# Kernel tuning notes

Hardware: AMD Instinct MI355X
Metric: run time of the kernel (lower is better)

The kernel has to match this reference:

```python
import jax, jax.numpy as jnp
import numpy as np

N = 50000
E = 800000
IN_CH = 256
HID = 32
HEADS = 4
OUT_CH = 40
NEG_SLOPE = 0.2
BN_EPS = 1e-5


def _gat_conv(x, W, att_src, att_dst, bias, src, dst, num_nodes, concat):
    # x: [N, F_in]; W: [F_in, H*C]; att_src/att_dst: [H, C]
    H, C = att_src.shape
    h = (x @ W).reshape(num_nodes, H, C)            # [N, H, C]
    a_src = (h * att_src[None]).sum(-1)             # [N, H]
    a_dst = (h * att_dst[None]).sum(-1)             # [N, H]
    e = jax.nn.leaky_relu(a_src[src] + a_dst[dst], NEG_SLOPE)  # [Etot, H]
    # segment softmax over incoming edges of each destination node
    m = jax.ops.segment_max(e, dst, num_segments=num_nodes)    # [N, H]
    ex = jnp.exp(e - m[dst])
    s = jax.ops.segment_sum(ex, dst, num_segments=num_nodes)   # [N, H]
    alpha = ex / (s[dst] + 1e-16)                   # [Etot, H]
    out = jax.ops.segment_sum(h[src] * alpha[:, :, None], dst,
                              num_segments=num_nodes)          # [N, H, C]
    out = out.reshape(num_nodes, H * C) if concat else out.mean(axis=1)
    return out + bias


def setup_inputs() -> dict:
    key = jax.random.key(0)
    ks = jax.random.split(key, 12)
    x = jax.random.normal(ks[0], (N, IN_CH), dtype=jnp.float32)
    edge_index = jax.random.randint(ks[1], (2, E), 0, N, dtype=jnp.int64)
    # layer 1: in -> heads*hid, concat
    W1 = jax.random.normal(ks[2], (IN_CH, HEADS * HID), dtype=jnp.float32) * (1.0 / np.sqrt(IN_CH))
    att_src1 = jax.random.normal(ks[3], (HEADS, HID), dtype=jnp.float32) * 0.1
    att_dst1 = jax.random.normal(ks[4], (HEADS, HID), dtype=jnp.float32) * 0.1
    b1 = jnp.zeros((HEADS * HID,), dtype=jnp.float32)
    # batch norm over hidden*heads features
    gamma = jnp.ones((HEADS * HID,), dtype=jnp.float32)
    beta = jnp.zeros((HEADS * HID,), dtype=jnp.float32)
    # layer 2: heads*hid -> out, heads=1, mean (concat=False)
    W2 = jax.random.normal(ks[5], (HEADS * HID, OUT_CH), dtype=jnp.float32) * (1.0 / np.sqrt(HEADS * HID))
    att_src2 = jax.random.normal(ks[6], (1, OUT_CH), dtype=jnp.float32) * 0.1
    att_dst2 = jax.random.normal(ks[7], (1, OUT_CH), dtype=jnp.float32) * 0.1
    b2 = jnp.zeros((OUT_CH,), dtype=jnp.float32)
    return {"x": x, "edge_index": edge_index, "W1": W1, "att_src1": att_src1,
            "att_dst1": att_dst1, "b1": b1, "gamma": gamma, "beta": beta,
            "W2": W2, "att_src2": att_src2, "att_dst2": att_dst2, "b2": b2}


def reference(x, edge_index, W1, att_src1, att_dst1, b1, gamma, beta,
              W2, att_src2, att_dst2, b2):
    num_nodes = x.shape[0]
    loops = jnp.arange(num_nodes, dtype=edge_index.dtype)
    src = jnp.concatenate([edge_index[0], loops])   # add self-loops (PyG default)
    dst = jnp.concatenate([edge_index[1], loops])
    h = _gat_conv(x, W1, att_src1, att_dst1, b1, src, dst, num_nodes, concat=True)
    # BatchNorm over nodes (training-mode batch statistics)
    mu = h.mean(axis=0)
    var = h.var(axis=0)
    h = (h - mu) * jax.lax.rsqrt(var + BN_EPS) * gamma + beta
    h = jax.nn.elu(h)
    out = _gat_conv(h, W2, att_src2, att_dst2, b2, src, dst, num_nodes, concat=False)
    return out
```

## Files before the change

### kernel.cpp

```cpp
#include <hip/hip_runtime.h>

#define NN 50000
#define EE 800000
#define FIN 256
#define F1 128
#define F2 40
#define CAP 48
#define G1B ((NN + 63) / 64)
#define FILLB ((EE + 255) / 256)
#define G1PB 3126
#define G2P0 3125
#define G2P1 ((NN + 63) / 64)
#define LSTR 56

typedef unsigned int u32;
typedef unsigned short u16;
typedef _Float16 h8 __attribute__((ext_vector_type(8)));
typedef float f4 __attribute__((ext_vector_type(4)));

static __device__ __forceinline__ u32 f2bf(float f) {
  u32 u = __float_as_uint(f);
  return (u + 0x7FFFu + ((u >> 16) & 1u)) >> 16;
}
#define BF_LO(u) __uint_as_float((u) << 16)
#define BF_HI(u) __uint_as_float((u) & 0xFFFF0000u)

static __device__ __forceinline__ int sel4i(int a, int b, int c, int d, int k) {
  int lo = (k & 1) ? b : a;
  int hi = (k & 1) ? d : c;
  return (k & 2) ? hi : lo;
}

__global__ __launch_bounds__(256) void g1f_kernel(const float* __restrict__ x,
                                                  const float* __restrict__ W1,
                                                  const float* __restrict__ att_src,
                                                  const float* __restrict__ att_dst,
                                                  u32* __restrict__ h1bf,
                                                  float* __restrict__ a_src,
                                                  float* __restrict__ a_dst,
                                                  const int* __restrict__ ei,
                                                  int* __restrict__ cnt,
                                                  u16* __restrict__ csr) {
  __shared__ __align__(16) _Float16 Alds[64 * LSTR];
  __shared__ __align__(16) _Float16 Blds[128 * LSTR];
  const int t = threadIdx.x;

  if (blockIdx.x >= G1B) {
    int e = (blockIdx.x - G1B) * 256 + t;
    if (e < EE) {
      int src = ei[e];
      int dst = ei[EE + e];
      int p = atomicAdd(cnt + dst, 1);
      if (p < CAP) csr[dst * CAP + p] = (u16)src;
    }
    return;
  }

  const int m0 = blockIdx.x * 64;
  const int l  = t & 63;
  const int w  = t >> 6;
  const int q  = l & 15;
  const int hq = l >> 4;

  const int arow  = t >> 2;
  const int akoff = (t & 3) * 8;
  const int bn    = t & 127;
  const int bkh   = (t >> 7) * 16;

  f4 acc[8] = {};

  float ax[8];
  float bx[16];
  {
    int gr = m0 + arow;
    if (gr < NN) {
      float4 u0 = *(const float4*)(x + (size_t)gr * FIN + akoff);
      float4 u1 = *(const float4*)(x + (size_t)gr * FIN + akoff + 4);
      ax[0] = u0.x; ax[1] = u0.y; ax[2] = u0.z; ax[3] = u0.w;
      ax[4] = u1.x; ax[5] = u1.y; ax[6] = u1.z; ax[7] = u1.w;
    } else {
#pragma unroll
      for (int i = 0; i < 8; ++i) ax[i] = 0.f;
    }
#pragma unroll
    for (int i = 0; i < 16; ++i) bx[i] = W1[(size_t)(bkh + i) * F1 + bn];
  }

  for (int s = 0; s < 8; ++s) {
    __syncthreads();
    {
      h8 av;
#pragma unroll
      for (int i = 0; i < 8; ++i) av[i] = (_Float16)ax[i];
      *(h8*)(Alds + arow * LSTR + akoff) = av;
      h8 bv0, bv1;
#pragma unroll
      for (int i = 0; i < 8; ++i) { bv0[i] = (_Float16)bx[i]; bv1[i] = (_Float16)bx[8 + i]; }
      *(h8*)(Blds + bn * LSTR + bkh) = bv0;
      *(h8*)(Blds + bn * LSTR + bkh + 8) = bv1;
    }
    __syncthreads();
    if (s < 7) {
      int k0 = (s + 1) * 32;
      int gr = m0 + arow;
      if (gr < NN) {
        float4 u0 = *(const float4*)(x + (size_t)gr * FIN + k0 + akoff);
        float4 u1 = *(const float4*)(x + (size_t)gr * FIN + k0 + akoff + 4);
        ax[0] = u0.x; ax[1] = u0.y; ax[2] = u0.z; ax[3] = u0.w;
        ax[4] = u1.x; ax[5] = u1.y; ax[6] = u1.z; ax[7] = u1.w;
      } else {
#pragma unroll
        for (int i = 0; i < 8; ++i) ax[i] = 0.f;
      }
#pragma unroll
      for (int i = 0; i < 16; ++i) bx[i] = W1[(size_t)(k0 + bkh + i) * F1 + bn];
    }
    h8 af = *(const h8*)(Alds + (w * 16 + q) * LSTR + hq * 8);
#pragma unroll
    for (int nf = 0; nf < 8; ++nf) {
      h8 bf = *(const h8*)(Blds + (nf * 16 + q) * LSTR + hq * 8);
      acc[nf] = __builtin_amdgcn_mfma_f32_16x16x32_f16(af, bf, acc[nf], 0, 0, 0);
    }
  }

  u16* h1u = (u16*)h1bf;
#pragma unroll
  for (int nf = 0; nf < 8; ++nf) {
    int ph = nf >> 1;
#pragma unroll
    for (int r = 0; r < 4; ++r) {
      int grow = m0 + w * 16 + hq * 4 + r;
      if (grow < NN)
        h1u[((size_t)ph * NN + grow) * 32 + (nf & 1) * 16 + q] = (u16)f2bf(acc[nf][r]);
    }
  }
  float as8[8], ad8[8];
#pragma unroll
  for (int nf = 0; nf < 8; ++nf) {
    as8[nf] = att_src[nf * 16 + q];
    ad8[nf] = att_dst[nf * 16 + q];
  }
#pragma unroll
  for (int r = 0; r < 4; ++r) {
    float p0 = acc[0][r] * as8[0] + acc[1][r] * as8[1];
    float p1 = acc[2][r] * as8[2] + acc[3][r] * as8[3];
    float p2 = acc[4][r] * as8[4] + acc[5][r] * as8[5];
    float p3 = acc[6][r] * as8[6] + acc[7][r] * as8[7];
    float d0 = acc[0][r] * ad8[0] + acc[1][r] * ad8[1];
    float d1 = acc[2][r] * ad8[2] + acc[3][r] * ad8[3];
    float d2 = acc[4][r] * ad8[4] + acc[5][r] * ad8[5];
    float d3 = acc[6][r] * ad8[6] + acc[7][r] * ad8[7];
#pragma unroll
    for (int off = 1; off < 16; off <<= 1) {
      p0 += __shfl_xor(p0, off); p1 += __shfl_xor(p1, off);
      p2 += __shfl_xor(p2, off); p3 += __shfl_xor(p3, off);
      d0 += __shfl_xor(d0, off); d1 += __shfl_xor(d1, off);
      d2 += __shfl_xor(d2, off); d3 += __shfl_xor(d3, off);
    }
    int grow = m0 + w * 16 + hq * 4 + r;
    if (grow < NN && q < 8) {
      float vs = (q & 2) ? ((q & 1) ? p3 : p2) : ((q & 1) ? p1 : p0);
      float vd = (q & 2) ? ((q & 1) ? d3 : d2) : ((q & 1) ? d1 : d0);
      if (q < 4) a_src[grow * 4 + q] = vs;
      else       a_dst[grow * 4 + (q - 4)] = vd;
    }
  }
}

__global__ __launch_bounds__(256) void gather1_kernel(const int* __restrict__ cnt,
                                                      const u16* __restrict__ csr,
                                                      const float* __restrict__ a_src,
                                                      const float* __restrict__ a_dst,
                                                      const u32* __restrict__ h1bf,
                                                      const float* __restrict__ b1,
                                                      float* __restrict__ h1b,
                                                      float* __restrict__ bnsum,
                                                      float* __restrict__ bnsq) {
  __shared__ float bns[32], bnq[32];
  __shared__ __align__(16) u16 idx[16 * CAP];
  int t = threadIdx.x;
  if (t < 32) { bns[t] = 0.f; bnq[t] = 0.f; }
  int d = blockIdx.x;
  int xcd = d & 7;
  int p = xcd >> 1;
  int nb = ((d >> 3) << 1) + (xcd & 1);
  int base_n = nb * 16;
  bool blk_ok = (nb < 3125);
  if (blk_ok && t < 96)
    ((uint4*)idx)[t] = ((const uint4*)(csr + (size_t)base_n * CAP))[t];
  __syncthreads();
  int n = base_n + (t >> 4);
  int sub = t & 15;
  int g = sub >> 2;
  int l = sub & 3;
  int f0 = p * 32 + l * 8;
  float acc[8] = {0.f, 0.f, 0.f, 0.f, 0.f, 0.f, 0.f, 0.f};
  float ssum = 0.f;
  if (blk_ok) {
    float adst = a_dst[n * 4 + p];
    const u32* hb = h1bf + (size_t)p * NN * 16 + l * 4;
    if (g == 0) {
      float e0 = a_src[n * 4 + p] + adst;
      e0 = e0 > 0.f ? e0 : 0.2f * e0;
      float x0 = __expf(e0);
      uint4 qv = *(const uint4*)(hb + (size_t)n * 16);
      acc[0] = fmaf(x0, BF_LO(qv.x), acc[0]); acc[1] = fmaf(x0, BF_HI(qv.x), acc[1]);
      acc[2] = fmaf(x0, BF_LO(qv.y), acc[2]); acc[3] = fmaf(x0, BF_HI(qv.y), acc[3]);
      acc[4] = fmaf(x0, BF_LO(qv.z), acc[4]); acc[5] = fmaf(x0, BF_HI(qv.z), acc[5]);
      acc[6] = fmaf(x0, BF_LO(qv.w), acc[6]); acc[7] = fmaf(x0, BF_HI(qv.w), acc[7]);
      ssum += x0;
    }
    const u16* lrow = idx + (t >> 4) * CAP;
    int m = cnt[n]; if (m > CAP) m = CAP;
    int sp = (m + 3) >> 2;
    int i = g * sp;
    int end = i + sp; if (end > m) end = m;
    int gb = (t & 63) & ~3;
    for (; i + 3 < end; i += 4) {
      int s0 = lrow[i + 0];
      int s1 = lrow[i + 1];
      int s2 = lrow[i + 2];
      int s3 = lrow[i + 3];
      float av = a_src[sel4i(s0, s1, s2, s3, l) * 4 + p];
      uint4 q0 = *(const uint4*)(hb + (size_t)s0 * 16);
      uint4 q1 = *(const uint4*)(hb + (size_t)s1 * 16);
      uint4 q2 = *(const uint4*)(hb + (size_t)s2 * 16);
      uint4 q3 = *(const uint4*)(hb + (size_t)s3 * 16);
      float e0 = __shfl(av, gb + 0, 64) + adst;
      float e1 = __shfl(av, gb + 1, 64) + adst;
      float e2 = __shfl(av, gb + 2, 64) + adst;
      float e3 = __shfl(av, gb + 3, 64) + adst;
      e0 = e0 > 0.f ? e0 : 0.2f * e0;  float x0 = __expf(e0);
      e1 = e1 > 0.f ? e1 : 0.2f * e1;  float x1 = __expf(e1);
      e2 = e2 > 0.f ? e2 : 0.2f * e2;  float x2 = __expf(e2);
      e3 = e3 > 0.f ? e3 : 0.2f * e3;  float x3 = __expf(e3);
      acc[0] = fmaf(x0, BF_LO(q0.x), acc[0]); acc[1] = fmaf(x0, BF_HI(q0.x), acc[1]);
      acc[2] = fmaf(x0, BF_LO(q0.y), acc[2]); acc[3] = fmaf(x0, BF_HI(q0.y), acc[3]);
      acc[4] = fmaf(x0, BF_LO(q0.z), acc[4]); acc[5] = fmaf(x0, BF_HI(q0.z), acc[5]);
      acc[6] = fmaf(x0, BF_LO(q0.w), acc[6]); acc[7] = fmaf(x0, BF_HI(q0.w), acc[7]);
      acc[0] = fmaf(x1, BF_LO(q1.x), acc[0]); acc[1] = fmaf(x1, BF_HI(q1.x), acc[1]);
      acc[2] = fmaf(x1, BF_LO(q1.y), acc[2]); acc[3] = fmaf(x1, BF_HI(q1.y), acc[3]);
      acc[4] = fmaf(x1, BF_LO(q1.z), acc[4]); acc[5] = fmaf(x1, BF_HI(q1.z), acc[5]);
      acc[6] = fmaf(x1, BF_LO(q1.w), acc[6]); acc[7] = fmaf(x1, BF_HI(q1.w), acc[7]);
      acc[0] = fmaf(x2, BF_LO(q2.x), acc[0]); acc[1] = fmaf(x2, BF_HI(q2.x), acc[1]);
      acc[2] = fmaf(x2, BF_LO(q2.y), acc[2]); acc[3] = fmaf(x2, BF_HI(q2.y), acc[3]);
      acc[4] = fmaf(x2, BF_LO(q2.z), acc[4]); acc[5] = fmaf(x2, BF_HI(q2.z), acc[5]);
      acc[6] = fmaf(x2, BF_LO(q2.w), acc[6]); acc[7] = fmaf(x2, BF_HI(q2.w), acc[7]);
      acc[0] = fmaf(x3, BF_LO(q3.x), acc[0]); acc[1] = fmaf(x3, BF_HI(q3.x), acc[1]);
      acc[2] = fmaf(x3, BF_LO(q3.y), acc[2]); acc[3] = fmaf(x3, BF_HI(q3.y), acc[3]);
      acc[4] = fmaf(x3, BF_LO(q3.z), acc[4]); acc[5] = fmaf(x3, BF_HI(q3.z), acc[5]);
      acc[6] = fmaf(x3, BF_LO(q3.w), acc[6]); acc[7] = fmaf(x3, BF_HI(q3.w), acc[7]);
      ssum += x0 + x1 + x2 + x3;
    }
    for (; i < end; ++i) {
      int s0 = lrow[i];
      float e0 = a_src[s0 * 4 + p] + adst;
      e0 = e0 > 0.f ? e0 : 0.2f * e0;
      float x0 = __expf(e0);
      uint4 qv = *(const uint4*)(hb + (size_t)s0 * 16);
      acc[0] = fmaf(x0, BF_LO(qv.x), acc[0]); acc[1] = fmaf(x0, BF_HI(qv.x), acc[1]);
      acc[2] = fmaf(x0, BF_LO(qv.y), acc[2]); acc[3] = fmaf(x0, BF_HI(qv.y), acc[3]);
      acc[4] = fmaf(x0, BF_LO(qv.z), acc[4]); acc[5] = fmaf(x0, BF_HI(qv.z), acc[5]);
      acc[6] = fmaf(x0, BF_LO(qv.w), acc[6]); acc[7] = fmaf(x0, BF_HI(qv.w), acc[7]);
      ssum += x0;
    }
  }
#pragma unroll
  for (int j = 0; j < 8; ++j) {
    acc[j] += __shfl_xor(acc[j], 4);
    acc[j] += __shfl_xor(acc[j], 8);
  }
  ssum += __shfl_xor(ssum, 4);
  ssum += __shfl_xor(ssum, 8);
  if (blk_ok && g == 0) {
    float inv = 1.f / (ssum + 1e-16f);
    float4 b0 = *(const float4*)(b1 + f0);
    float4 b4 = *(const float4*)(b1 + f0 + 4);
    float o[8];
    o[0] = acc[0] * inv + b0.x; o[1] = acc[1] * inv + b0.y;
    o[2] = acc[2] * inv + b0.z; o[3] = acc[3] * inv + b0.w;
    o[4] = acc[4] * inv + b4.x; o[5] = acc[5] * inv + b4.y;
    o[6] = acc[6] * inv + b4.z; o[7] = acc[7] * inv + b4.w;
    float4 w0 = {o[0], o[1], o[2], o[3]};
    float4 w1 = {o[4], o[5], o[6], o[7]};
    *(float4*)(h1b + (size_t)n * F1 + f0) = w0;
    *(float4*)(h1b + (size_t)n * F1 + f0 + 4) = w1;
    int lb = l * 8;
#pragma unroll
    for (int j = 0; j < 8; ++j) {
      atomicAdd(&bns[lb + j], o[j]);
      atomicAdd(&bnq[lb + j], o[j] * o[j]);
    }
  }
  __syncthreads();
  if (t < 32) {
    atomicAdd(bnsum + p * 32 + t, bns[t]);
    atomicAdd(bnsq + p * 32 + t, bnq[t]);
  }
}

__global__ __launch_bounds__(256) void gemm2_kernel(const float* __restrict__ hpre,
                                                    const float* __restrict__ W2,
                                                    const float* __restrict__ bnsum,
                                                    const float* __restrict__ bnsq,
                                                    const float* __restrict__ gamma,
                                                    const float* __restrict__ beta,
                                                    u16* __restrict__ h2a,
                                                    u16* __restrict__ h2b,
                                                    const float* __restrict__ att_src2,
                                                    const float* __restrict__ att_dst2,
                                                    float* __restrict__ a_src2,
                                                    float* __restrict__ a_dst2) {
  __shared__ float Wlds[128 * 40];
  __shared__ float Alds[16 * 128];
  __shared__ float sc[128], sh[128];
  int t = threadIdx.x;
  for (int i = t; i < 128 * 40; i += 256) Wlds[i] = W2[i];
  if (t < 128) {
    const float invN = 1.f / (float)NN;
    float mu = bnsum[t] * invN;
    float var = bnsq[t] * invN - mu * mu;
    float s = gamma[t] * rsqrtf(var + 1e-5f);
    sc[t] = s;
    sh[t] = beta[t] - mu * s;
  }
  int tr = t >> 3;
  int tc = t & 7;
  float as5[5], ad5[5];
#pragma unroll
  for (int j = 0; j < 5; ++j) { as5[j] = att_src2[tc * 5 + j]; ad5[j] = att_dst2[tc * 5 + j]; }
  int n0 = blockIdx.x * 128;
  int lrow = t >> 1;
  int lkk = (t & 1) * 8;
  float acc[4][5];
#pragma unroll
  for (int i = 0; i < 4; ++i)
#pragma unroll
    for (int j = 0; j < 5; ++j) acc[i][j] = 0.f;

  for (int k0 = 0; k0 < F1; k0 += 16) {
    float av[8];
    int gn = n0 + lrow;
    if (gn < NN) {
      float4 v0 = *(const float4*)(hpre + (size_t)gn * F1 + k0 + lkk);
      float4 v1 = *(const float4*)(hpre + (size_t)gn * F1 + k0 + lkk + 4);
      av[0] = v0.x; av[1] = v0.y; av[2] = v0.z; av[3] = v0.w;
      av[4] = v1.x; av[5] = v1.y; av[6] = v1.z; av[7] = v1.w;
    } else {
#pragma unroll
      for (int j = 0; j < 8; ++j) av[j] = 0.f;
    }
    __syncthreads();
#pragma unroll
    for (int j = 0; j < 8; ++j) {
      int kg = k0 + lkk + j;
      float a = av[j] * sc[kg] + sh[kg];
      a = a > 0.f ? a : (__expf(a) - 1.f);
      Alds[(lkk + j) * 128 + lrow] = a;
    }
    __syncthreads();
#pragma unroll
    for (int k = 0; k < 16; ++k) {
      float4 a4 = *(const float4*)(Alds + k * 128 + tr * 4);
      float aa[4] = {a4.x, a4.y, a4.z, a4.w};
      float w[5];
#pragma unroll
      for (int j = 0; j < 5; ++j) w[j] = Wlds[(k0 + k) * 40 + tc * 5 + j];
#pragma unroll
      for (int i = 0; i < 4; ++i)
#pragma unroll
        for (int j = 0; j < 5; ++j) acc[i][j] = fmaf(aa[i], w[j], acc[i][j]);
    }
  }
#pragma unroll
  for (int i = 0; i < 4; ++i) {
    int gn = n0 + tr * 4 + i;
    if (gn < NN) {
#pragma unroll
      for (int j = 0; j < 5; ++j) {
        int f = tc * 5 + j;
        u16 v = (u16)f2bf(acc[i][j]);
        if (f < 32) h2a[(size_t)gn * 32 + f] = v;
        else        h2b[(size_t)gn * 8 + (f - 32)] = v;
      }
    }
  }
#pragma unroll
  for (int i = 0; i < 4; ++i) {
    float ps = 0.f, pd = 0.f;
#pragma unroll
    for (int j = 0; j < 5; ++j) { ps += acc[i][j] * as5[j]; pd += acc[i][j] * ad5[j]; }
#pragma unroll
    for (int off = 1; off < 8; off <<= 1) {
      ps += __shfl_xor(ps, off);
      pd += __shfl_xor(pd, off);
    }
    if (tc == 0) {
      int gn = n0 + tr * 4 + i;
      if (gn < NN) { a_src2[gn] = ps; a_dst2[gn] = pd; }
    }
  }
}

__global__ __launch_bounds__(256) void gather2_kernel(const int* __restrict__ cnt,
                                                      const u16* __restrict__ csr,
                                                      const float* __restrict__ a_src,
                                                      const float* __restrict__ a_dst,
                                                      const u32* __restrict__ h2a,
                                                      const u32* __restrict__ h2b,
                                                      const float* __restrict__ b2,
                                                      float* __restrict__ out) {
  int t = threadIdx.x;
  int d = blockIdx.x;
  if (d < G2P0) {
    __shared__ __align__(16) u16 idx[16 * CAP];
    int base_n = d * 16;
    if (t < 96)
      ((uint4*)idx)[t] = ((const uint4*)(csr + (size_t)base_n * CAP))[t];
    __syncthreads();
    int n = base_n + (t >> 4);
    int sub = t & 15;
    int g = sub >> 2;
    int l = sub & 3;
    float adst = a_dst[n];
    const u32* hb = h2a + l * 4;
    float acc[8] = {0.f, 0.f, 0.f, 0.f, 0.f, 0.f, 0.f, 0.f};
    float ssum = 0.f;
    if (g == 0) {
      float e0 = a_src[n] + adst;
      e0 = e0 > 0.f ? e0 : 0.2f * e0;
      float x0 = __expf(e0);
      uint4 qv = *(const uint4*)(hb + (size_t)n * 16);
      acc[0] = fmaf(x0, BF_LO(qv.x), acc[0]); acc[1] = fmaf(x0, BF_HI(qv.x), acc[1]);
      acc[2] = fmaf(x0, BF_LO(qv.y), acc[2]); acc[3] = fmaf(x0, BF_HI(qv.y), acc[3]);
      acc[4] = fmaf(x0, BF_LO(qv.z), acc[4]); acc[5] = fmaf(x0, BF_HI(qv.z), acc[5]);
      acc[6] = fmaf(x0, BF_LO(qv.w), acc[6]); acc[7] = fmaf(x0, BF_HI(qv.w), acc[7]);
      ssum += x0;
    }
    const u16* lrow = idx + (t >> 4) * CAP;
    int m = cnt[n]; if (m > CAP) m = CAP;
    int sp = (m + 3) >> 2;
    int i = g * sp;
    int end = i + sp; if (end > m) end = m;
    int gb = (t & 63) & ~3;
    for (; i + 3 < end; i += 4) {
      int s0 = lrow[i + 0];
      int s1 = lrow[i + 1];
      int s2 = lrow[i + 2];
      int s3 = lrow[i + 3];
      float av = a_src[sel4i(s0, s1, s2, s3, l)];
      uint4 q0 = *(const uint4*)(hb + (size_t)s0 * 16);
      uint4 q1 = *(const uint4*)(hb + (size_t)s1 * 16);
      uint4 q2 = *(const uint4*)(hb + (size_t)s2 * 16);
      uint4 q3 = *(const uint4*)(hb + (size_t)s3 * 16);
      float e0 = __shfl(av, gb + 0, 64) + adst;
      float e1 = __shfl(av, gb + 1, 64) + adst;
      float e2 = __shfl(av, gb + 2, 64) + adst;
      float e3 = __shfl(av, gb + 3, 64) + adst;
      e0 = e0 > 0.f ? e0 : 0.2f * e0;  float x0 = __expf(e0);
      e1 = e1 > 0.f ? e1 : 0.2f * e1;  float x1 = __expf(e1);
      e2 = e2 > 0.f ? e2 : 0.2f * e2;  float x2 = __expf(e2);
      e3 = e3 > 0.f ? e3 : 0.2f * e3;  float x3 = __expf(e3);
      acc[0] = fmaf(x0, BF_LO(q0.x), acc[0]); acc[1] = fmaf(x0, BF_HI(q0.x), acc[1]);
      acc[2] = fmaf(x0, BF_LO(q0.y), acc[2]); acc[3] = fmaf(x0, BF_HI(q0.y), acc[3]);
      acc[4] = fmaf(x0, BF_LO(q0.z), acc[4]); acc[5] = fmaf(x0, BF_HI(q0.z), acc[5]);
      acc[6] = fmaf(x0, BF_LO(q0.w), acc[6]); acc[7] = fmaf(x0, BF_HI(q0.w), acc[7]);
      acc[0] = fmaf(x1, BF_LO(q1.x), acc[0]); acc[1] = fmaf(x1, BF_HI(q1.x), acc[1]);
      acc[2] = fmaf(x1, BF_LO(q1.y), acc[2]); acc[3] = fmaf(x1, BF_HI(q1.y), acc[3]);
      acc[4] = fmaf(x1, BF_LO(q1.z), acc[4]); acc[5] = fmaf(x1, BF_HI(q1.z), acc[5]);
      acc[6] = fmaf(x1, BF_LO(q1.w), acc[6]); acc[7] = fmaf(x1, BF_HI(q1.w), acc[7]);
      acc[0] = fmaf(x2, BF_LO(q2.x), acc[0]); acc[1] = fmaf(x2, BF_HI(q2.x), acc[1]);
      acc[2] = fmaf(x2, BF_LO(q2.y), acc[2]); acc[3] = fmaf(x2, BF_HI(q2.y), acc[3]);
      acc[4] = fmaf(x2, BF_LO(q2.z), acc[4]); acc[5] = fmaf(x2, BF_HI(q2.z), acc[5]);
      acc[6] = fmaf(x2, BF_LO(q2.w), acc[6]); acc[7] = fmaf(x2, BF_HI(q2.w), acc[7]);
      acc[0] = fmaf(x3, BF_LO(q3.x), acc[0]); acc[1] = fmaf(x3, BF_HI(q3.x), acc[1]);
      acc[2] = fmaf(x3, BF_LO(q3.y), acc[2]); acc[3] = fmaf(x3, BF_HI(q3.y), acc[3]);
      acc[4] = fmaf(x3, BF_LO(q3.z), acc[4]); acc[5] = fmaf(x3, BF_HI(q3.z), acc[5]);
      acc[6] = fmaf(x3, BF_LO(q3.w), acc[6]); acc[7] = fmaf(x3, BF_HI(q3.w), acc[7]);
      ssum += x0 + x1 + x2 + x3;
    }
    for (; i < end; ++i) {
      int s0 = lrow[i];
      float e0 = a_src[s0] + adst;
      e0 = e0 > 0.f ? e0 : 0.2f * e0;
      float x0 = __expf(e0);
      uint4 qv = *(const uint4*)(hb + (size_t)s0 * 16);
      acc[0] = fmaf(x0, BF_LO(qv.x), acc[0]); acc[1] = fmaf(x0, BF_HI(qv.x), acc[1]);
      acc[2] = fmaf(x0, BF_LO(qv.y), acc[2]); acc[3] = fmaf(x0, BF_HI(qv.y), acc[3]);
      acc[4] = fmaf(x0, BF_LO(qv.z), acc[4]); acc[5] = fmaf(x0, BF_HI(qv.z), acc[5]);
      acc[6] = fmaf(x0, BF_LO(qv.w), acc[6]); acc[7] = fmaf(x0, BF_HI(qv.w), acc[7]);
      ssum += x0;
    }
#pragma unroll
    for (int j = 0; j < 8; ++j) {
      acc[j] += __shfl_xor(acc[j], 4);
      acc[j] += __shfl_xor(acc[j], 8);
    }
    ssum += __shfl_xor(ssum, 4);
    ssum += __shfl_xor(ssum, 8);
    if (g == 0) {
      float inv = 1.f / (ssum + 1e-16f);
      int f0 = l * 8;
      float4 b0 = *(const float4*)(b2 + f0);
      float4 b4 = *(const float4*)(b2 + f0 + 4);
      float4 w0 = {acc[0] * inv + b0.x, acc[1] * inv + b0.y,
                   acc[2] * inv + b0.z, acc[3] * inv + b0.w};
      float4 w1 = {acc[4] * inv + b4.x, acc[5] * inv + b4.y,
                   acc[6] * inv + b4.z, acc[7] * inv + b4.w};
      *(float4*)(out + (size_t)n * F2 + f0) = w0;
      *(float4*)(out + (size_t)n * F2 + f0 + 4) = w1;
    }
  } else {
    int n = (d - G2P0) * 64 + (t >> 2);
    int g = t & 3;
    float acc[8] = {0.f, 0.f, 0.f, 0.f, 0.f, 0.f, 0.f, 0.f};
    float ssum = 0.f;
    if (n < NN) {
      float adst = a_dst[n];
      if (g == 0) {
        float e0 = a_src[n] + adst;
        e0 = e0 > 0.f ? e0 : 0.2f * e0;
        float x0 = __expf(e0);
        uint4 qv = *(const uint4*)(h2b + (size_t)n * 4);
        acc[0] = fmaf(x0, BF_LO(qv.x), acc[0]); acc[1] = fmaf(x0, BF_HI(qv.x), acc[1]);
        acc[2] = fmaf(x0, BF_LO(qv.y), acc[2]); acc[3] = fmaf(x0, BF_HI(qv.y), acc[3]);
        acc[4] = fmaf(x0, BF_LO(qv.z), acc[4]); acc[5] = fmaf(x0, BF_HI(qv.z), acc[5]);
        acc[6] = fmaf(x0, BF_LO(qv.w), acc[6]); acc[7] = fmaf(x0, BF_HI(qv.w), acc[7]);
        ssum += x0;
      }
      const u16* row = csr + (size_t)n * CAP;
      int m = cnt[n]; if (m > CAP) m = CAP;
      int i = g;
      for (; i + 4 < m; i += 8) {
        int s0 = row[i];
        int s1 = row[i + 4];
        float e0 = a_src[s0];
        float e1 = a_src[s1];
        uint4 q0 = *(const uint4*)(h2b + (size_t)s0 * 4);
        uint4 q1 = *(const uint4*)(h2b + (size_t)s1 * 4);
        e0 += adst; e0 = e0 > 0.f ? e0 : 0.2f * e0;  float x0 = __expf(e0);
        e1 += adst; e1 = e1 > 0.f ? e1 : 0.2f * e1;  float x1 = __expf(e1);
        acc[0] = fmaf(x0, BF_LO(q0.x), acc[0]); acc[1] = fmaf(x0, BF_HI(q0.x), acc[1]);
        acc[2] = fmaf(x0, BF_LO(q0.y), acc[2]); acc[3] = fmaf(x0, BF_HI(q0.y), acc[3]);
        acc[4] = fmaf(x0, BF_LO(q0.z), acc[4]); acc[5] = fmaf(x0, BF_HI(q0.z), acc[5]);
        acc[6] = fmaf(x0, BF_LO(q0.w), acc[6]); acc[7] = fmaf(x0, BF_HI(q0.w), acc[7]);
        acc[0] = fmaf(x1, BF_LO(q1.x), acc[0]); acc[1] = fmaf(x1, BF_HI(q1.x), acc[1]);
        acc[2] = fmaf(x1, BF_LO(q1.y), acc[2]); acc[3] = fmaf(x1, BF_HI(q1.y), acc[3]);
        acc[4] = fmaf(x1, BF_LO(q1.z), acc[4]); acc[5] = fmaf(x1, BF_HI(q1.z), acc[5]);
        acc[6] = fmaf(x1, BF_LO(q1.w), acc[6]); acc[7] = fmaf(x1, BF_HI(q1.w), acc[7]);
        ssum += x0 + x1;
      }
      for (; i < m; i += 4) {
        int s0 = row[i];
        float e0 = a_src[s0] + adst;
        e0 = e0 > 0.f ? e0 : 0.2f * e0;
        float x0 = __expf(e0);
        uint4 qv = *(const uint4*)(h2b + (size_t)s0 * 4);
        acc[0] = fmaf(x0, BF_LO(qv.x), acc[0]); acc[1] = fmaf(x0, BF_HI(qv.x), acc[1]);
        acc[2] = fmaf(x0, BF_LO(qv.y), acc[2]); acc[3] = fmaf(x0, BF_HI(qv.y), acc[3]);
        acc[4] = fmaf(x0, BF_LO(qv.z), acc[4]); acc[5] = fmaf(x0, BF_HI(qv.z), acc[5]);
        acc[6] = fmaf(x0, BF_LO(qv.w), acc[6]); acc[7] = fmaf(x0, BF_HI(qv.w), acc[7]);
        ssum += x0;
      }
    }
#pragma unroll
    for (int j = 0; j < 8; ++j) {
      acc[j] += __shfl_xor(acc[j], 1);
      acc[j] += __shfl_xor(acc[j], 2);
    }
    ssum += __shfl_xor(ssum, 1);
    ssum += __shfl_xor(ssum, 2);
    if (n < NN && g == 0) {
      float inv = 1.f / (ssum + 1e-16f);
      float4 b0 = *(const float4*)(b2 + 32);
      float4 b4 = *(const float4*)(b2 + 36);
      float4 w0 = {acc[0] * inv + b0.x, acc[1] * inv + b0.y,
                   acc[2] * inv + b0.z, acc[3] * inv + b0.w};
      float4 w1 = {acc[4] * inv + b4.x, acc[5] * inv + b4.y,
                   acc[6] * inv + b4.z, acc[7] * inv + b4.w};
      *(float4*)(out + (size_t)n * F2 + 32) = w0;
      *(float4*)(out + (size_t)n * F2 + 36) = w1;
    }
  }
}

extern "C" void kernel_launch(void* const* d_in, const int* in_sizes, int n_in,
                              void* d_out, int out_size, void* d_ws, size_t ws_size,
                              hipStream_t stream) {
  const float* x        = (const float*)d_in[0];
  const int*   ei       = (const int*)d_in[1];
  const float* W1       = (const float*)d_in[2];
  const float* att_src1 = (const float*)d_in[3];
  const float* att_dst1 = (const float*)d_in[4];
  const float* b1       = (const float*)d_in[5];
  const float* gamma    = (const float*)d_in[6];
  const float* beta     = (const float*)d_in[7];
  const float* W2       = (const float*)d_in[8];
  const float* att_src2 = (const float*)d_in[9];
  const float* att_dst2 = (const float*)d_in[10];
  const float* b2       = (const float*)d_in[11];
  float* out = (float*)d_out;

  int* cnt      = (int*)d_ws;
  float* bnsum  = (float*)(cnt + 50048);
  float* bnsq   = bnsum + 128;
  u16* csr      = (u16*)(bnsq + 128);
  u32* h1bf     = (u32*)(csr + (size_t)NN * CAP);
  float* h1b    = (float*)(h1bf + 3200000);
  u32* h2a      = (u32*)(h1b + 6400000);
  u32* h2b      = h2a + 800000;
  float* a_src1 = (float*)(h2b + 200000);
  float* a_dst1 = a_src1 + 200000;
  float* a_src2 = a_dst1 + 200000;
  float* a_dst2 = a_src2 + 50000;

  hipMemsetAsync(cnt, 0, (50048 + 256) * sizeof(int), stream);

  g1f_kernel<<<G1B + FILLB, 256, 0, stream>>>(x, W1, att_src1, att_dst1,
                                              h1bf, a_src1, a_dst1,
                                              ei, cnt, csr);
  gather1_kernel<<<(G1PB / 2) * 8, 256, 0, stream>>>(cnt, csr, a_src1, a_dst1,
                                                     h1bf, b1, h1b, bnsum, bnsq);
  gemm2_kernel<<<(NN + 127) / 128, 256, 0, stream>>>(h1b, W2, bnsum, bnsq,
                                                     gamma, beta,
                                                     (u16*)h2a, (u16*)h2b,
                                                     att_src2, att_dst2,
                                                     a_src2, a_dst2);
  gather2_kernel<<<G2P0 + G2P1, 256, 0, stream>>>(cnt, csr, a_src2, a_dst2,
                                                  h2a, h2b, b2, out);
}
```

Before: 287.8 us.

## Merge second-layer gather paths and pack tail features with source attention score

The second-layer gather previously ran two separate block populations: one covering the first 32 output features and one covering the last 8, each walking the CSR rows and recomputing attention weights. It now uses a single pass in which each lane also loads a 32-byte record holding the 8 tail features plus the a_src score, and accumulates those tail features alongside the main ones. This removes the duplicate edge traversal, exp computation and extra blocks, and replaces a separate a_src gather with a load that also brings in the tail features. In exchange, per-thread register use and memory traffic grow slightly, and a layout is added that stores the score inside the bf16 row padding.

```diff
diff --git a/kernel.cpp b/kernel.cpp
--- a/kernel.cpp
+++ b/kernel.cpp
@@ -9,8 +9,7 @@
 #define G1B ((NN + 63) / 64)
 #define FILLB ((EE + 255) / 256)
 #define G1PB 3126
-#define G2P0 3125
-#define G2P1 ((NN + 63) / 64)
+#define G2B 3125
 #define LSTR 56
 
 typedef unsigned int u32;
@@ -28,6 +27,11 @@
 static __device__ __forceinline__ int sel4i(int a, int b, int c, int d, int k) {
   int lo = (k & 1) ? b : a;
   int hi = (k & 1) ? d : c;
+  return (k & 2) ? hi : lo;
+}
+static __device__ __forceinline__ float sel4f(float a, float b, float c, float d, int k) {
+  float lo = (k & 1) ? b : a;
+  float hi = (k & 1) ? d : c;
   return (k & 2) ? hi : lo;
 }
 
@@ -306,10 +310,9 @@
                                                     const float* __restrict__ gamma,
                                                     const float* __restrict__ beta,
                                                     u16* __restrict__ h2a,
-                                                    u16* __restrict__ h2b,
+                                                    u16* __restrict__ h2x,
                                                     const float* __restrict__ att_src2,
                                                     const float* __restrict__ att_dst2,
-                                                    float* __restrict__ a_src2,
                                                     float* __restrict__ a_dst2) {
   __shared__ float Wlds[128 * 40];
   __shared__ float Alds[16 * 128];
@@ -381,7 +384,7 @@
         int f = tc * 5 + j;
         u16 v = (u16)f2bf(acc[i][j]);
         if (f < 32) h2a[(size_t)gn * 32 + f] = v;
-        else        h2b[(size_t)gn * 8 + (f - 32)] = v;
+        else        h2x[(size_t)gn * 16 + (f - 32)] = v;
       }
     }
   }
@@ -397,189 +400,159 @@
     }
     if (tc == 0) {
       int gn = n0 + tr * 4 + i;
-      if (gn < NN) { a_src2[gn] = ps; a_dst2[gn] = pd; }
+      if (gn < NN) {
+        a_dst2[gn] = pd;
+        *(float*)(h2x + (size_t)gn * 16 + 8) = ps;
+      }
     }
   }
 }
 
 __global__ __launch_bounds__(256) void gather2_kernel(const int* __restrict__ cnt,
                                                       const u16* __restrict__ csr,
-                                                      const float* __restrict__ a_src,
                                                       const float* __restrict__ a_dst,
                                                       const u32* __restrict__ h2a,
-                                                      const u32* __restrict__ h2b,
+                                                      const u32* __restrict__ h2x,
                                                       const float* __restrict__ b2,
                                                       float* __restrict__ out) {
+  __shared__ __align__(16) u16 idx[16 * CAP];
   int t = threadIdx.x;
-  int d = blockIdx.x;
-  if (d < G2P0) {
-    __shared__ __align__(16) u16 idx[16 * CAP];
-    int base_n = d * 16;
-    if (t < 96)
-      ((uint4*)idx)[t] = ((const uint4*)(csr + (size_t)base_n * CAP))[t];
-    __syncthreads();
-    int n = base_n + (t >> 4);
-    int sub = t & 15;
-    int g = sub >> 2;
-    int l = sub & 3;
-    float adst = a_dst[n];
-    const u32* hb = h2a + l * 4;
-    float acc[8] = {0.f, 0.f, 0.f, 0.f, 0.f, 0.f, 0.f, 0.f};
-    float ssum = 0.f;
-    if (g == 0) {
-      float e0 = a_src[n] + adst;
-      e0 = e0 > 0.f ? e0 : 0.2f * e0;
-      float x0 = __expf(e0);
-      uint4 qv = *(const uint4*)(hb + (size_t)n * 16);
-      acc[0] = fmaf(x0, BF_LO(qv.x), acc[0]); acc[1] = fmaf(x0, BF_HI(qv.x), acc[1]);
-      acc[2] = fmaf(x0, BF_LO(qv.y), acc[2]); acc[3] = fmaf(x0, BF_HI(qv.y), acc[3]);
-      acc[4] = fmaf(x0, BF_LO(qv.z), acc[4]); acc[5] = fmaf(x0, BF_HI(qv.z), acc[5]);
-      acc[6] = fmaf(x0, BF_LO(qv.w), acc[6]); acc[7] = fmaf(x0, BF_HI(qv.w), acc[7]);
-      ssum += x0;
-    }
-    const u16* lrow = idx + (t >> 4) * CAP;
-    int m = cnt[n]; if (m > CAP) m = CAP;
-    int sp = (m + 3) >> 2;
-    int i = g * sp;
-    int end = i + sp; if (end > m) end = m;
-    int gb = (t & 63) & ~3;
-    for (; i + 3 < end; i += 4) {
-      int s0 = lrow[i + 0];
-      int s1 = lrow[i + 1];
-      int s2 = lrow[i + 2];
-      int s3 = lrow[i + 3];
-      float av = a_src[sel4i(s0, s1, s2, s3, l)];
-      uint4 q0 = *(const uint4*)(hb + (size_t)s0 * 16);
-      uint4 q1 = *(const uint4*)(hb + (size_t)s1 * 16);
-      uint4 q2 = *(const uint4*)(hb + (size_t)s2 * 16);
-      uint4 q3 = *(const uint4*)(hb + (size_t)s3 * 16);
-      float e0 = __shfl(av, gb + 0, 64) + adst;
-      float e1 = __shfl(av, gb + 1, 64) + adst;
-      float e2 = __shfl(av, gb + 2, 64) + adst;
-      float e3 = __shfl(av, gb + 3, 64) + adst;
-      e0 = e0 > 0.f ? e0 : 0.2f * e0;  float x0 = __expf(e0);
-      e1 = e1 > 0.f ? e1 : 0.2f * e1;  float x1 = __expf(e1);
-      e2 = e2 > 0.f ? e2 : 0.2f * e2;  float x2 = __expf(e2);
-      e3 = e3 > 0.f ? e3 : 0.2f * e3;  float x3 = __expf(e3);
-      acc[0] = fmaf(x0, BF_LO(q0.x), acc[0]); acc[1] = fmaf(x0, BF_HI(q0.x), acc[1]);
-      acc[2] = fmaf(x0, BF_LO(q0.y), acc[2]); acc[3] = fmaf(x0, BF_HI(q0.y), acc[3]);
-      acc[4] = fmaf(x0, BF_LO(q0.z), acc[4]); acc[5] = fmaf(x0, BF_HI(q0.z), acc[5]);
-      acc[6] = fmaf(x0, BF_LO(q0.w), acc[6]); acc[7] = fmaf(x0, BF_HI(q0.w), acc[7]);
-      acc[0] = fmaf(x1, BF_LO(q1.x), acc[0]); acc[1] = fmaf(x1, BF_HI(q1.x), acc[1]);
-      acc[2] = fmaf(x1, BF_LO(q1.y), acc[2]); acc[3] = fmaf(x1, BF_HI(q1.y), acc[3]);
-      acc[4] = fmaf(x1, BF_LO(q1.z), acc[4]); acc[5] = fmaf(x1, BF_HI(q1.z), acc[5]);
-      acc[6] = fmaf(x1, BF_LO(q1.w), acc[6]); acc[7] = fmaf(x1, BF_HI(q1.w), acc[7]);
-      acc[0] = fmaf(x2, BF_LO(q2.x), acc[0]); acc[1] = fmaf(x2, BF_HI(q2.x), acc[1]);
-      acc[2] = fmaf(x2, BF_LO(q2.y), acc[2]); acc[3] = fmaf(x2, BF_HI(q2.y), acc[3]);
-      acc[4] = fmaf(x2, BF_LO(q2.z), acc[4]); acc[5] = fmaf(x2, BF_HI(q2.z), acc[5]);
-      acc[6] = fmaf(x2, BF_LO(q2.w), acc[6]); acc[7] = fmaf(x2, BF_HI(q2.w), acc[7]);
-      acc[0] = fmaf(x3, BF_LO(q3.x), acc[0]); acc[1] = fmaf(x3, BF_HI(q3.x), acc[1]);
-      acc[2] = fmaf(x3, BF_LO(q3.y), acc[2]); acc[3] = fmaf(x3, BF_HI(q3.y), acc[3]);
-      acc[4] = fmaf(x3, BF_LO(q3.z), acc[4]); acc[5] = fmaf(x3, BF_HI(q3.z), acc[5]);
-      acc[6] = fmaf(x3, BF_LO(q3.w), acc[6]); acc[7] = fmaf(x3, BF_HI(q3.w), acc[7]);
-      ssum += x0 + x1 + x2 + x3;
-    }
-    for (; i < end; ++i) {
-      int s0 = lrow[i];
-      float e0 = a_src[s0] + adst;
-      e0 = e0 > 0.f ? e0 : 0.2f * e0;
-      float x0 = __expf(e0);
-      uint4 qv = *(const uint4*)(hb + (size_t)s0 * 16);
-      acc[0] = fmaf(x0, BF_LO(qv.x), acc[0]); acc[1] = fmaf(x0, BF_HI(qv.x), acc[1]);
-      acc[2] = fmaf(x0, BF_LO(qv.y), acc[2]); acc[3] = fmaf(x0, BF_HI(qv.y), acc[3]);
-      acc[4] = fmaf(x0, BF_LO(qv.z), acc[4]); acc[5] = fmaf(x0, BF_HI(qv.z), acc[5]);
-      acc[6] = fmaf(x0, BF_LO(qv.w), acc[6]); acc[7] = fmaf(x0, BF_HI(qv.w), acc[7]);
-      ssum += x0;
-    }
-#pragma unroll
-    for (int j = 0; j < 8; ++j) {
-      acc[j] += __shfl_xor(acc[j], 4);
-      acc[j] += __shfl_xor(acc[j], 8);
-    }
-    ssum += __shfl_xor(ssum, 4);
-    ssum += __shfl_xor(ssum, 8);
-    if (g == 0) {
-      float inv = 1.f / (ssum + 1e-16f);
-      int f0 = l * 8;
-      float4 b0 = *(const float4*)(b2 + f0);
-      float4 b4 = *(const float4*)(b2 + f0 + 4);
-      float4 w0 = {acc[0] * inv + b0.x, acc[1] * inv + b0.y,
-                   acc[2] * inv + b0.z, acc[3] * inv + b0.w};
-      float4 w1 = {acc[4] * inv + b4.x, acc[5] * inv + b4.y,
-                   acc[6] * inv + b4.z, acc[7] * inv + b4.w};
-      *(float4*)(out + (size_t)n * F2 + f0) = w0;
-      *(float4*)(out + (size_t)n * F2 + f0 + 4) = w1;
-    }
-  } else {
-    int n = (d - G2P0) * 64 + (t >> 2);
-    int g = t & 3;
-    float acc[8] = {0.f, 0.f, 0.f, 0.f, 0.f, 0.f, 0.f, 0.f};
-    float ssum = 0.f;
-    if (n < NN) {
-      float adst = a_dst[n];
-      if (g == 0) {
-        float e0 = a_src[n] + adst;
-        e0 = e0 > 0.f ? e0 : 0.2f * e0;
-        float x0 = __expf(e0);
-        uint4 qv = *(const uint4*)(h2b + (size_t)n * 4);
-        acc[0] = fmaf(x0, BF_LO(qv.x), acc[0]); acc[1] = fmaf(x0, BF_HI(qv.x), acc[1]);
-        acc[2] = fmaf(x0, BF_LO(qv.y), acc[2]); acc[3] = fmaf(x0, BF_HI(qv.y), acc[3]);
-        acc[4] = fmaf(x0, BF_LO(qv.z), acc[4]); acc[5] = fmaf(x0, BF_HI(qv.z), acc[5]);
-        acc[6] = fmaf(x0, BF_LO(qv.w), acc[6]); acc[7] = fmaf(x0, BF_HI(qv.w), acc[7]);
-        ssum += x0;
-      }
-      const u16* row = csr + (size_t)n * CAP;
-      int m = cnt[n]; if (m > CAP) m = CAP;
-      int i = g;
-      for (; i + 4 < m; i += 8) {
-        int s0 = row[i];
-        int s1 = row[i + 4];
-        float e0 = a_src[s0];
-        float e1 = a_src[s1];
-        uint4 q0 = *(const uint4*)(h2b + (size_t)s0 * 4);
-        uint4 q1 = *(const uint4*)(h2b + (size_t)s1 * 4);
-        e0 += adst; e0 = e0 > 0.f ? e0 : 0.2f * e0;  float x0 = __expf(e0);
-        e1 += adst; e1 = e1 > 0.f ? e1 : 0.2f * e1;  float x1 = __expf(e1);
-        acc[0] = fmaf(x0, BF_LO(q0.x), acc[0]); acc[1] = fmaf(x0, BF_HI(q0.x), acc[1]);
-        acc[2] = fmaf(x0, BF_LO(q0.y), acc[2]); acc[3] = fmaf(x0, BF_HI(q0.y), acc[3]);
-        acc[4] = fmaf(x0, BF_LO(q0.z), acc[4]); acc[5] = fmaf(x0, BF_HI(q0.z), acc[5]);
-        acc[6] = fmaf(x0, BF_LO(q0.w), acc[6]); acc[7] = fmaf(x0, BF_HI(q0.w), acc[7]);
-        acc[0] = fmaf(x1, BF_LO(q1.x), acc[0]); acc[1] = fmaf(x1, BF_HI(q1.x), acc[1]);
-        acc[2] = fmaf(x1, BF_LO(q1.y), acc[2]); acc[3] = fmaf(x1, BF_HI(q1.y), acc[3]);
-        acc[4] = fmaf(x1, BF_LO(q1.z), acc[4]); acc[5] = fmaf(x1, BF_HI(q1.z), acc[5]);
-        acc[6] = fmaf(x1, BF_LO(q1.w), acc[6]); acc[7] = fmaf(x1, BF_HI(q1.w), acc[7]);
-        ssum += x0 + x1;
-      }
-      for (; i < m; i += 4) {
-        int s0 = row[i];
-        float e0 = a_src[s0] + adst;
-        e0 = e0 > 0.f ? e0 : 0.2f * e0;
-        float x0 = __expf(e0);
-        uint4 qv = *(const uint4*)(h2b + (size_t)s0 * 4);
-        acc[0] = fmaf(x0, BF_LO(qv.x), acc[0]); acc[1] = fmaf(x0, BF_HI(qv.x), acc[1]);
-        acc[2] = fmaf(x0, BF_LO(qv.y), acc[2]); acc[3] = fmaf(x0, BF_HI(qv.y), acc[3]);
-        acc[4] = fmaf(x0, BF_LO(qv.z), acc[4]); acc[5] = fmaf(x0, BF_HI(qv.z), acc[5]);
-        acc[6] = fmaf(x0, BF_LO(qv.w), acc[6]); acc[7] = fmaf(x0, BF_HI(qv.w), acc[7]);
-        ssum += x0;
-      }
-    }
-#pragma unroll
-    for (int j = 0; j < 8; ++j) {
-      acc[j] += __shfl_xor(acc[j], 1);
-      acc[j] += __shfl_xor(acc[j], 2);
-    }
-    ssum += __shfl_xor(ssum, 1);
-    ssum += __shfl_xor(ssum, 2);
-    if (n < NN && g == 0) {
-      float inv = 1.f / (ssum + 1e-16f);
-      float4 b0 = *(const float4*)(b2 + 32);
-      float4 b4 = *(const float4*)(b2 + 36);
-      float4 w0 = {acc[0] * inv + b0.x, acc[1] * inv + b0.y,
-                   acc[2] * inv + b0.z, acc[3] * inv + b0.w};
-      float4 w1 = {acc[4] * inv + b4.x, acc[5] * inv + b4.y,
-                   acc[6] * inv + b4.z, acc[7] * inv + b4.w};
-      *(float4*)(out + (size_t)n * F2 + 32) = w0;
-      *(float4*)(out + (size_t)n * F2 + 36) = w1;
+  int base_n = blockIdx.x * 16;
+  if (t < 96)
+    ((uint4*)idx)[t] = ((const uint4*)(csr + (size_t)base_n * CAP))[t];
+  __syncthreads();
+  int n = base_n + (t >> 4);
+  int sub = t & 15;
+  int g = sub >> 2;
+  int l = sub & 3;
+  float adst = a_dst[n];
+  const u32* hb = h2a + l * 4;
+  float acc[8]  = {0.f, 0.f, 0.f, 0.f, 0.f, 0.f, 0.f, 0.f};
+  float accx[8] = {0.f, 0.f, 0.f, 0.f, 0.f, 0.f, 0.f, 0.f};
+  float ssum = 0.f;
+  if (g == 0) {
+    const u32* xr = h2x + (size_t)n * 8;
+    float e0 = __uint_as_float(xr[4]) + adst;
+    e0 = e0 > 0.f ? e0 : 0.2f * e0;
+    float x0 = __expf(e0);
+    uint4 qv = *(const uint4*)(hb + (size_t)n * 16);
+    acc[0] = fmaf(x0, BF_LO(qv.x), acc[0]); acc[1] = fmaf(x0, BF_HI(qv.x), acc[1]);
+    acc[2] = fmaf(x0, BF_LO(qv.y), acc[2]); acc[3] = fmaf(x0, BF_HI(qv.y), acc[3]);
+    acc[4] = fmaf(x0, BF_LO(qv.z), acc[4]); acc[5] = fmaf(x0, BF_HI(qv.z), acc[5]);
+    acc[6] = fmaf(x0, BF_LO(qv.w), acc[6]); acc[7] = fmaf(x0, BF_HI(qv.w), acc[7]);
+    if (l == 0) {
+      uint4 xf = *(const uint4*)xr;
+      accx[0] = fmaf(x0, BF_LO(xf.x), accx[0]); accx[1] = fmaf(x0, BF_HI(xf.x), accx[1]);
+      accx[2] = fmaf(x0, BF_LO(xf.y), accx[2]); accx[3] = fmaf(x0, BF_HI(xf.y), accx[3]);
+      accx[4] = fmaf(x0, BF_LO(xf.z), accx[4]); accx[5] = fmaf(x0, BF_HI(xf.z), accx[5]);
+      accx[6] = fmaf(x0, BF_LO(xf.w), accx[6]); accx[7] = fmaf(x0, BF_HI(xf.w), accx[7]);
+    }
+    ssum += x0;
+  }
+  const u16* lrow = idx + (t >> 4) * CAP;
+  int m = cnt[n]; if (m > CAP) m = CAP;
+  int sp = (m + 3) >> 2;
+  int i = g * sp;
+  int end = i + sp; if (end > m) end = m;
+  int gb = (t & 63) & ~3;
+  for (; i + 3 < end; i += 4) {
+    int s0 = lrow[i + 0];
+    int s1 = lrow[i + 1];
+    int s2 = lrow[i + 2];
+    int s3 = lrow[i + 3];
+    int sl = sel4i(s0, s1, s2, s3, l);
+    const u32* xr = h2x + (size_t)sl * 8;
+    uint4 xf = *(const uint4*)xr;
+    float asv = __uint_as_float(xr[4]);
+    uint4 q0 = *(const uint4*)(hb + (size_t)s0 * 16);
+    uint4 q1 = *(const uint4*)(hb + (size_t)s1 * 16);
+    uint4 q2 = *(const uint4*)(hb + (size_t)s2 * 16);
+    uint4 q3 = *(const uint4*)(hb + (size_t)s3 * 16);
+    float e0 = __shfl(asv, gb + 0, 64) + adst;
+    float e1 = __shfl(asv, gb + 1, 64) + adst;
+    float e2 = __shfl(asv, gb + 2, 64) + adst;
+    float e3 = __shfl(asv, gb + 3, 64) + adst;
+    e0 = e0 > 0.f ? e0 : 0.2f * e0;  float x0 = __expf(e0);
+    e1 = e1 > 0.f ? e1 : 0.2f * e1;  float x1 = __expf(e1);
+    e2 = e2 > 0.f ? e2 : 0.2f * e2;  float x2 = __expf(e2);
+    e3 = e3 > 0.f ? e3 : 0.2f * e3;  float x3 = __expf(e3);
+    acc[0] = fmaf(x0, BF_LO(q0.x), acc[0]); acc[1] = fmaf(x0, BF_HI(q0.x), acc[1]);
+    acc[2] = fmaf(x0, BF_LO(q0.y), acc[2]); acc[3] = fmaf(x0, BF_HI(q0.y), acc[3]);
+    acc[4] = fmaf(x0, BF_LO(q0.z), acc[4]); acc[5] = fmaf(x0, BF_HI(q0.z), acc[5]);
+    acc[6] = fmaf(x0, BF_LO(q0.w), acc[6]); acc[7] = fmaf(x0, BF_HI(q0.w), acc[7]);
+    acc[0] = fmaf(x1, BF_LO(q1.x), acc[0]); acc[1] = fmaf(x1, BF_HI(q1.x), acc[1]);
+    acc[2] = fmaf(x1, BF_LO(q1.y), acc[2]); acc[3] = fmaf(x1, BF_HI(q1.y), acc[3]);
+    acc[4] = fmaf(x1, BF_LO(q1.z), acc[4]); acc[5] = fmaf(x1, BF_HI(q1.z), acc[5]);
+    acc[6] = fmaf(x1, BF_LO(q1.w), acc[6]); acc[7] = fmaf(x1, BF_HI(q1.w), acc[7]);
+    acc[0] = fmaf(x2, BF_LO(q2.x), acc[0]); acc[1] = fmaf(x2, BF_HI(q2.x), acc[1]);
+    acc[2] = fmaf(x2, BF_LO(q2.y), acc[2]); acc[3] = fmaf(x2, BF_HI(q2.y), acc[3]);
+    acc[4] = fmaf(x2, BF_LO(q2.z), acc[4]); acc[5] = fmaf(x2, BF_HI(q2.z), acc[5]);
+    acc[6] = fmaf(x2, BF_LO(q2.w), acc[6]); acc[7] = fmaf(x2, BF_HI(q2.w), acc[7]);
+    acc[0] = fmaf(x3, BF_LO(q3.x), acc[0]); acc[1] = fmaf(x3, BF_HI(q3.x), acc[1]);
+    acc[2] = fmaf(x3, BF_LO(q3.y), acc[2]); acc[3] = fmaf(x3, BF_HI(q3.y), acc[3]);
+    acc[4] = fmaf(x3, BF_LO(q3.z), acc[4]); acc[5] = fmaf(x3, BF_HI(q3.z), acc[5]);
+    acc[6] = fmaf(x3, BF_LO(q3.w), acc[6]); acc[7] = fmaf(x3, BF_HI(q3.w), acc[7]);
+    float xl = sel4f(x0, x1, x2, x3, l);
+    accx[0] = fmaf(xl, BF_LO(xf.x), accx[0]); accx[1] = fmaf(xl, BF_HI(xf.x), accx[1]);
+    accx[2] = fmaf(xl, BF_LO(xf.y), accx[2]); accx[3] = fmaf(xl, BF_HI(xf.y), accx[3]);
+    accx[4] = fmaf(xl, BF_LO(xf.z), accx[4]); accx[5] = fmaf(xl, BF_HI(xf.z), accx[5]);
+    accx[6] = fmaf(xl, BF_LO(xf.w), accx[6]); accx[7] = fmaf(xl, BF_HI(xf.w), accx[7]);
+    ssum += x0 + x1 + x2 + x3;
+  }
+  for (; i < end; ++i) {
+    int s0 = lrow[i];
+    const u32* xr = h2x + (size_t)s0 * 8;
+    float e0 = __uint_as_float(xr[4]) + adst;
+    e0 = e0 > 0.f ? e0 : 0.2f * e0;
+    float x0 = __expf(e0);
+    uint4 qv = *(const uint4*)(hb + (size_t)s0 * 16);
+    acc[0] = fmaf(x0, BF_LO(qv.x), acc[0]); acc[1] = fmaf(x0, BF_HI(qv.x), acc[1]);
+    acc[2] = fmaf(x0, BF_LO(qv.y), acc[2]); acc[3] = fmaf(x0, BF_HI(qv.y), acc[3]);
+    acc[4] = fmaf(x0, BF_LO(qv.z), acc[4]); acc[5] = fmaf(x0, BF_HI(qv.z), acc[5]);
+    acc[6] = fmaf(x0, BF_LO(qv.w), acc[6]); acc[7] = fmaf(x0, BF_HI(qv.w), acc[7]);
+    if (l == 0) {
+      uint4 xf = *(const uint4*)xr;
+      accx[0] = fmaf(x0, BF_LO(xf.x), accx[0]); accx[1] = fmaf(x0, BF_HI(xf.x), accx[1]);
+      accx[2] = fmaf(x0, BF_LO(xf.y), accx[2]); accx[3] = fmaf(x0, BF_HI(xf.y), accx[3]);
+      accx[4] = fmaf(x0, BF_LO(xf.z), accx[4]); accx[5] = fmaf(x0, BF_HI(xf.z), accx[5]);
+      accx[6] = fmaf(x0, BF_LO(xf.w), accx[6]); accx[7] = fmaf(x0, BF_HI(xf.w), accx[7]);
+    }
+    ssum += x0;
+  }
+#pragma unroll
+  for (int j = 0; j < 8; ++j) {
+    accx[j] += __shfl_xor(accx[j], 1);
+    accx[j] += __shfl_xor(accx[j], 2);
+  }
+#pragma unroll
+  for (int j = 0; j < 8; ++j) {
+    acc[j]  += __shfl_xor(acc[j], 4);
+    acc[j]  += __shfl_xor(acc[j], 8);
+    accx[j] += __shfl_xor(accx[j], 4);
+    accx[j] += __shfl_xor(accx[j], 8);
+  }
+  ssum += __shfl_xor(ssum, 4);
+  ssum += __shfl_xor(ssum, 8);
+  float inv = 1.f / (ssum + 1e-16f);
+  if (g == 0) {
+    int f0 = l * 8;
+    float4 b0 = *(const float4*)(b2 + f0);
+    float4 b4 = *(const float4*)(b2 + f0 + 4);
+    float4 w0 = {acc[0] * inv + b0.x, acc[1] * inv + b0.y,
+                 acc[2] * inv + b0.z, acc[3] * inv + b0.w};
+    float4 w1 = {acc[4] * inv + b4.x, acc[5] * inv + b4.y,
+                 acc[6] * inv + b4.z, acc[7] * inv + b4.w};
+    *(float4*)(out + (size_t)n * F2 + f0) = w0;
+    *(float4*)(out + (size_t)n * F2 + f0 + 4) = w1;
+    if (l == 0) {
+      float4 c0 = *(const float4*)(b2 + 32);
+      float4 c4 = *(const float4*)(b2 + 36);
+      float4 v0 = {accx[0] * inv + c0.x, accx[1] * inv + c0.y,
+                   accx[2] * inv + c0.z, accx[3] * inv + c0.w};
+      float4 v1 = {accx[4] * inv + c4.x, accx[5] * inv + c4.y,
+                   accx[6] * inv + c4.z, accx[7] * inv + c4.w};
+      *(float4*)(out + (size_t)n * F2 + 32) = v0;
+      *(float4*)(out + (size_t)n * F2 + 36) = v1;
     }
   }
 }
@@ -608,11 +581,10 @@
   u32* h1bf     = (u32*)(csr + (size_t)NN * CAP);
   float* h1b    = (float*)(h1bf + 3200000);
   u32* h2a      = (u32*)(h1b + 6400000);
-  u32* h2b      = h2a + 800000;
-  float* a_src1 = (float*)(h2b + 200000);
+  u32* h2x      = h2a + 800000;
+  float* a_src1 = (float*)(h2x + 400000);
   float* a_dst1 = a_src1 + 200000;
-  float* a_src2 = a_dst1 + 200000;
-  float* a_dst2 = a_src2 + 50000;
+  float* a_dst2 = a_dst1 + 200000;
 
   hipMemsetAsync(cnt, 0, (50048 + 256) * sizeof(int), stream);
 
@@ -623,9 +595,9 @@
                                                      h1bf, b1, h1b, bnsum, bnsq);
   gemm2_kernel<<<(NN + 127) / 128, 256, 0, stream>>>(h1b, W2, bnsum, bnsq,
                                                      gamma, beta,
-                                                     (u16*)h2a, (u16*)h2b,
+                                                     (u16*)h2a, (u16*)h2x,
                                                      att_src2, att_dst2,
-                                                     a_src2, a_dst2);
-  gather2_kernel<<<G2P0 + G2P1, 256, 0, stream>>>(cnt, csr, a_src2, a_dst2,
-                                                  h2a, h2b, b2, out);
-}
+                                                     a_dst2);
+  gather2_kernel<<<G2B, 256, 0, stream>>>(cnt, csr, a_dst2,
+                                          h2a, h2x, b2, out);
+}
```

New measurement: 301.6 us. 4.8% more time.
